# Kernel tuning notes

Hardware: AMD Instinct MI355X
Metric: run time of the kernel (lower is better)

The kernel has to match this reference:

```python
import jax, jax.numpy as jnp
import numpy as np

BATCH = 4096
N_CTRL = 64      # num_control_points
ORDER = 3        # spline degree p
DIM = 3          # spatial dimension (channels = DIM + 1, last is weight)
OUT_DIM = 2048   # sampled points per curve


def _gen_knot_vector(order, num_control_points, delta=1e-06):
    m = order + num_control_points + 1
    num_segments = m - 2 * (order + 1) + 1
    kv = [(j + 1) * delta for j in range(order)]
    kv += list(np.linspace(delta * (order + 1), 1.0, num_segments + 1))
    kv += [1.0 for _ in range(order)]
    return np.asarray(kv, dtype=np.float64)


def _find_span(n, p, u, U):
    # n = num_ctrl - 1; returns span index in [p, n]
    if u >= U[n + 1]:
        return n
    if u <= U[p]:
        return p
    low, high = p, n + 1
    mid = (low + high) // 2
    while u < U[mid] or u >= U[mid + 1]:
        if u < U[mid]:
            high = mid
        else:
            low = mid
        mid = (low + high) // 2
    return mid


def _basis_funs(span, u, p, U):
    # Cox-de Boor recursion (NURBS book A2.2) -> p+1 nonzero basis values
    N = np.zeros(p + 1)
    N[0] = 1.0
    left = np.zeros(p + 1)
    right = np.zeros(p + 1)
    for j in range(1, p + 1):
        left[j] = u - U[span + 1 - j]
        right[j] = U[span + j] - u
        saved = 0.0
        for r in range(j):
            temp = N[r] / (right[r + 1] + left[j - r])
            N[r] = saved + right[r + 1] * temp
            saved = left[j - r] * temp
        N[j] = saved
    return N


def _precompute_basis():
    U = _gen_knot_vector(ORDER, N_CTRL)
    u_params = np.linspace(0.0, 1.0, OUT_DIM)
    n = N_CTRL - 1
    spans = np.empty(OUT_DIM, dtype=np.int32)
    basis = np.empty((OUT_DIM, ORDER + 1), dtype=np.float32)
    for i, u in enumerate(u_params):
        s = _find_span(n, ORDER, u, U)
        spans[i] = s
        basis[i] = _basis_funs(s, u, ORDER, U)
    return spans, basis


def setup_inputs() -> dict:
    key = jax.random.key(0)
    k_xyz, k_w = jax.random.split(key)
    xyz = jax.random.normal(k_xyz, (BATCH, N_CTRL, DIM), dtype=jnp.float32)
    # positive rational weights to keep the homogeneous divide well-conditioned
    w = jax.random.uniform(k_w, (BATCH, N_CTRL, 1), dtype=jnp.float32) + 0.5
    control_points = jnp.concatenate([xyz, w], axis=-1)  # [B, N, DIM+1]
    spans_np, basis_np = _precompute_basis()
    return {
        "control_points": control_points,
        "span": jnp.asarray(spans_np),          # [S] int32, values in [ORDER, N_CTRL-1]
        "basis": jnp.asarray(basis_np),         # [S, ORDER+1] float32
    }


def reference(control_points, span, basis):
    p = basis.shape[1] - 1
    dim = control_points.shape[-1] - 1
    # curves[b, s, :] = sum_j basis[s, j] * control_points[b, span[s] - p + j, :]
    curves = basis[:, 0][None, :, None] * control_points[:, span - p, :]
    for j in range(1, p + 1):
        curves = curves + basis[:, j][None, :, None] * control_points[:, span - p + j, :]
    # rational (homogeneous) divide
    return curves[:, :, :dim] / curves[:, :, dim][:, :, None]
```

## Files before the change

### kernel.cpp

```cpp
#include <hip/hip_runtime.h>

#define BATCH 4096
#define NCTRL 64
#define SDIM  2048
#define SBLK  256

__global__ __launch_bounds__(SBLK) void curve_eval_kernel(
    const float4* __restrict__ cp,
    const int*    __restrict__ span,
    const float4* __restrict__ basis,
    float4*       __restrict__ out)
{
    __shared__ float4 cp_s[NCTRL];
    __shared__ float  out_s[SBLK * 3];

    const int b   = blockIdx.y;
    const int s0  = blockIdx.x * SBLK;
    const int tid = threadIdx.x;

    if (tid < NCTRL) {
        cp_s[tid] = cp[(size_t)b * NCTRL + tid];
    }
    __syncthreads();

    const int s = s0 + tid;
    const int sp = span[s];
    const float4 bas = basis[s];

    const float4 r0 = cp_s[sp - 3];
    const float4 r1 = cp_s[sp - 2];
    const float4 r2 = cp_s[sp - 1];
    const float4 r3 = cp_s[sp - 0];

    float4 acc;
    acc.x = bas.x * r0.x + bas.y * r1.x + bas.z * r2.x + bas.w * r3.x;
    acc.y = bas.x * r0.y + bas.y * r1.y + bas.z * r2.y + bas.w * r3.y;
    acc.z = bas.x * r0.z + bas.y * r1.z + bas.z * r2.z + bas.w * r3.z;
    acc.w = bas.x * r0.w + bas.y * r1.w + bas.z * r2.w + bas.w * r3.w;

    const float invw = 1.0f / acc.w;
    out_s[tid * 3 + 0] = acc.x * invw;
    out_s[tid * 3 + 1] = acc.y * invw;
    out_s[tid * 3 + 2] = acc.z * invw;
    __syncthreads();

    const size_t base4 = ((size_t)b * SDIM + (size_t)s0) * 3u / 4u;
    if (tid < (SBLK * 3 / 4)) {
        const float4 v = reinterpret_cast<const float4*>(out_s)[tid];
        out[base4 + tid] = v;
    }
}

extern "C" void kernel_launch(void* const* d_in, const int* in_sizes, int n_in,
                              void* d_out, int out_size, void* d_ws, size_t ws_size,
                              hipStream_t stream) {
    const float4* cp    = (const float4*)d_in[0];
    const int*    span  = (const int*)d_in[1];
    const float4* basis = (const float4*)d_in[2];
    float4*       out   = (float4*)d_out;

    dim3 grid(SDIM / SBLK, BATCH);
    curve_eval_kernel<<<grid, SBLK, 0, stream>>>(cp, span, basis, out);
}
```

Before: 26.90 us.

## Process four samples per thread and use nontemporal vector stores

Each block now covers 1024 samples instead of 256. Every thread evaluates four samples, so the grid shrinks fourfold and each control-point tile staged in shared memory is reused across more outputs. The output write-back now has all threads store three float4s each with nontemporal hints, where before only 3/4 of the threads stored one. In exchange there are fewer blocks, more shared memory per block and more registers per thread.

```diff
diff --git a/kernel.cpp b/kernel.cpp
--- a/kernel.cpp
+++ b/kernel.cpp
@@ -4,18 +4,22 @@
 #define NCTRL 64
 #define SDIM  2048
 #define SBLK  256
+#define VPT   4
+#define CHUNK (SBLK * VPT)
+
+typedef float f32x4 __attribute__((ext_vector_type(4)));
 
 __global__ __launch_bounds__(SBLK) void curve_eval_kernel(
     const float4* __restrict__ cp,
     const int*    __restrict__ span,
     const float4* __restrict__ basis,
-    float4*       __restrict__ out)
+    f32x4*        __restrict__ out)
 {
     __shared__ float4 cp_s[NCTRL];
-    __shared__ float  out_s[SBLK * 3];
+    __shared__ float  out_s[CHUNK * 3];
 
     const int b   = blockIdx.y;
-    const int s0  = blockIdx.x * SBLK;
+    const int s0  = blockIdx.x * CHUNK;
     const int tid = threadIdx.x;
 
     if (tid < NCTRL) {
@@ -23,31 +27,36 @@
     }
     __syncthreads();
 
-    const int s = s0 + tid;
-    const int sp = span[s];
-    const float4 bas = basis[s];
+    #pragma unroll
+    for (int k = 0; k < VPT; ++k) {
+        const int ls = tid + k * SBLK;
+        const int s  = s0 + ls;
+        const int sp = span[s];
+        const float4 bas = basis[s];
 
-    const float4 r0 = cp_s[sp - 3];
-    const float4 r1 = cp_s[sp - 2];
-    const float4 r2 = cp_s[sp - 1];
-    const float4 r3 = cp_s[sp - 0];
+        const float4 r0 = cp_s[sp - 3];
+        const float4 r1 = cp_s[sp - 2];
+        const float4 r2 = cp_s[sp - 1];
+        const float4 r3 = cp_s[sp - 0];
 
-    float4 acc;
-    acc.x = bas.x * r0.x + bas.y * r1.x + bas.z * r2.x + bas.w * r3.x;
-    acc.y = bas.x * r0.y + bas.y * r1.y + bas.z * r2.y + bas.w * r3.y;
-    acc.z = bas.x * r0.z + bas.y * r1.z + bas.z * r2.z + bas.w * r3.z;
-    acc.w = bas.x * r0.w + bas.y * r1.w + bas.z * r2.w + bas.w * r3.w;
+        const float x = bas.x * r0.x + bas.y * r1.x + bas.z * r2.x + bas.w * r3.x;
+        const float y = bas.x * r0.y + bas.y * r1.y + bas.z * r2.y + bas.w * r3.y;
+        const float z = bas.x * r0.z + bas.y * r1.z + bas.z * r2.z + bas.w * r3.z;
+        const float w = bas.x * r0.w + bas.y * r1.w + bas.z * r2.w + bas.w * r3.w;
 
-    const float invw = 1.0f / acc.w;
-    out_s[tid * 3 + 0] = acc.x * invw;
-    out_s[tid * 3 + 1] = acc.y * invw;
-    out_s[tid * 3 + 2] = acc.z * invw;
+        const float invw = 1.0f / w;
+        out_s[ls * 3 + 0] = x * invw;
+        out_s[ls * 3 + 1] = y * invw;
+        out_s[ls * 3 + 2] = z * invw;
+    }
     __syncthreads();
 
+    const f32x4* out_s4 = reinterpret_cast<const f32x4*>(out_s);
     const size_t base4 = ((size_t)b * SDIM + (size_t)s0) * 3u / 4u;
-    if (tid < (SBLK * 3 / 4)) {
-        const float4 v = reinterpret_cast<const float4*>(out_s)[tid];
-        out[base4 + tid] = v;
+    #pragma unroll
+    for (int k = 0; k < 3; ++k) {
+        __builtin_nontemporal_store(out_s4[tid + k * SBLK],
+                                    &out[base4 + tid + k * SBLK]);
     }
 }
 
@@ -57,8 +66,8 @@
     const float4* cp    = (const float4*)d_in[0];
     const int*    span  = (const int*)d_in[1];
     const float4* basis = (const float4*)d_in[2];
-    float4*       out   = (float4*)d_out;
+    f32x4*        out   = (f32x4*)d_out;
 
-    dim3 grid(SDIM / SBLK, BATCH);
+    dim3 grid(SDIM / CHUNK, BATCH);
     curve_eval_kernel<<<grid, SBLK, 0, stream>>>(cp, span, basis, out);
 }
```

Result: slower. 29.43 us (+9.4%).
